# Performance work log

Measured on AMD Instinct MI355X. Metric: run time of the kernel, lower is better.

The kernel has to match this reference:

```python
import jax, jax.numpy as jnp
import numpy as np

B, S, D, H, HD = 4, 2048, 1024, 16, 64  # batch, seq, d_model, heads, head_dim


def setup_inputs() -> dict:
    key = jax.random.key(0)
    ks = jax.random.split(key, 9)
    scale = 0.02
    x = jax.random.normal(ks[0], (B, S, D), jnp.float32)
    Wq = jax.random.normal(ks[1], (D, H, HD), jnp.float32) * scale
    Wk = jax.random.normal(ks[2], (D, H, HD), jnp.float32) * scale
    Wv = jax.random.normal(ks[3], (D, H, HD), jnp.float32) * scale
    bq = jax.random.normal(ks[4], (H, HD), jnp.float32) * scale
    bk = jax.random.normal(ks[5], (H, HD), jnp.float32) * scale
    bv = jax.random.normal(ks[6], (H, HD), jnp.float32) * scale
    Wo = jax.random.normal(ks[7], (H, HD, D), jnp.float32) * scale
    bo = jax.random.normal(ks[8], (D,), jnp.float32) * scale
    return {"x": x, "Wq": Wq, "bq": bq, "Wk": Wk, "bk": bk,
            "Wv": Wv, "bv": bv, "Wo": Wo, "bo": bo}


def reference(x, Wq, bq, Wk, bk, Wv, bv, Wo, bo):
    # QKV projections -> (B, S, H, HD)
    q = jnp.einsum("bsd,dhe->bshe", x, Wq) + bq
    k = jnp.einsum("bsd,dhe->bshe", x, Wk) + bk
    v = jnp.einsum("bsd,dhe->bshe", x, Wv) + bv
    # scaled dot-product attention (deterministic, no mask/bias)
    q = q / jnp.sqrt(jnp.asarray(HD, q.dtype))
    scores = jnp.einsum("bqhd,bkhd->bhqk", q, k)  # (B, H, S, S)
    attn = jax.nn.softmax(scores, axis=-1)
    ctx = jnp.einsum("bhqk,bkhd->bqhd", attn, v)  # (B, S, H, HD)
    # output projection -> (B, S, D)
    return jnp.einsum("bqhd,hdo->bqo", ctx, Wo) + bo
```

## Files before the change

### kernel.cpp

```cpp
#include <hip/hip_runtime.h>


typedef unsigned short u16;
typedef __attribute__((ext_vector_type(4))) float f32x4;
typedef __attribute__((ext_vector_type(8))) short s16x8;
typedef __attribute__((ext_vector_type(4))) unsigned short u16x4;
typedef __attribute__((ext_vector_type(2))) unsigned int u32x2;
typedef __attribute__((ext_vector_type(4))) unsigned int u32x4;

#define DEV __device__ __forceinline__

#if __has_builtin(__builtin_amdgcn_exp2f)
#define EXP2(x) __builtin_amdgcn_exp2f(x)
#else
#define EXP2(x) exp2f(x)
#endif

DEV u16 f2b(float f) {
  unsigned u = __float_as_uint(f);
  u += 0x7fffu + ((u >> 16) & 1u);
  return (u16)(u >> 16);
}

DEV unsigned pack2(float a, float b) {
#if __has_builtin(__builtin_amdgcn_cvt_pk_bf16_f32)
  typedef __attribute__((ext_vector_type(2))) __bf16 bf16x2;
  bf16x2 r = __builtin_amdgcn_cvt_pk_bf16_f32(a, b);
  return __builtin_bit_cast(unsigned, r);
#else
  return (unsigned)f2b(a) | ((unsigned)f2b(b) << 16);
#endif
}

DEV void async16(const void* g, void* l) {
  __builtin_amdgcn_global_load_lds(
      (const __attribute__((address_space(1))) unsigned int*)g,
      (__attribute__((address_space(3))) unsigned int*)l, 16, 0, 0);
}

__global__ void k_cast(const float* __restrict__ x, u16* __restrict__ xb) {
  int i = (blockIdx.x * 256 + threadIdx.x) * 4;
  float4 v = *(const float4*)(x + i);
  u16x4 o;
  o.x = f2b(v.x); o.y = f2b(v.y); o.z = f2b(v.z); o.w = f2b(v.w);
  *(u16x4*)(xb + i) = o;
}

__global__ void k_packw_all(const float* __restrict__ Wq, const float* __restrict__ Wk,
                            const float* __restrict__ Wv, const float* __restrict__ Wo,
                            u16* __restrict__ wt, u16* __restrict__ wot, float qscale) {
  const float* src; u16* dst; float scale = 1.0f;
  switch (blockIdx.z) {
    case 0: src = Wq; dst = wt; scale = qscale; break;
    case 1: src = Wk; dst = wt + 1024 * 1024; break;
    case 2: src = Wv; dst = wt + 2 * 1024 * 1024; break;
    default: src = Wo; dst = wot; break;
  }
  __shared__ float tile[32][33];
  int t = threadIdx.x;
  int k0 = blockIdx.x * 32, n0 = blockIdx.y * 32;
  int c = t & 31, r0 = t >> 5;
#pragma unroll
  for (int p = 0; p < 4; ++p) {
    int r = p * 8 + r0;
    tile[r][c] = src[(size_t)(k0 + r) * 1024 + n0 + c] * scale;
  }
  __syncthreads();
#pragma unroll
  for (int p = 0; p < 4; ++p) {
    int r = p * 8 + r0;
    dst[(size_t)(n0 + r) * 1024 + k0 + c] = f2b(tile[c][r]);
  }
}

__global__ void k_packbias(const float* __restrict__ bq, const float* __restrict__ bk,
                           const float* __restrict__ bv, float* __restrict__ out,
                           float qscale) {
  int t = blockIdx.x * 256 + threadIdx.x;
  float v = (t < 1024) ? bq[t] * qscale : (t < 2048 ? bk[t - 1024] : bv[t - 2048]);
  out[t] = v;
}

template <int MODE>
__global__ __launch_bounds__(256, 2) void k_gemm_bt(
    const u16* __restrict__ A, const u16* __restrict__ Bt,
    const float* __restrict__ bias, void* __restrict__ Cout,
    int K, int ldC, int nbase) {
  __shared__ u16 As[128 * 64];
  __shared__ u16 Bs[128 * 64];
  const int t = threadIdx.x;
  const int w = t >> 6, l = t & 63;
  const int lane15 = l & 15, quad = l >> 4;
  const int m0 = blockIdx.x * 128, n0 = nbase + blockIdx.y * 128;
  const int wm = (w >> 1) * 64, wn = (w & 1) * 64;

  const int srow = t >> 3, cp = t & 7;
  const u16* aSrc[4]; const u16* bSrc[4]; int ldsOff[4];
#pragma unroll
  for (int i = 0; i < 4; ++i) {
    int row = i * 32 + srow;
    int gc = cp ^ (row & 7);
    aSrc[i] = A + (size_t)(m0 + row) * K + gc * 8;
    bSrc[i] = Bt + (size_t)(n0 + row) * K + gc * 8;
    ldsOff[i] = (i * 32 + w * 8) * 64;
  }

  f32x4 acc[4][4] = {};

  for (int kk = 0; kk < K; kk += 64) {
#pragma unroll
    for (int i = 0; i < 4; ++i) async16(aSrc[i] + kk, As + ldsOff[i]);
#pragma unroll
    for (int i = 0; i < 4; ++i) async16(bSrc[i] + kk, Bs + ldsOff[i]);
    __builtin_amdgcn_s_waitcnt(0);
    __syncthreads();

#pragma unroll
    for (int ks = 0; ks < 2; ++ks) {
      s16x8 af[4], bf[4];
#pragma unroll
      for (int mi = 0; mi < 4; ++mi) {
        int r = wm + mi * 16 + lane15;
        int c = ks * 4 + quad;
        af[mi] = *(const s16x8*)(As + r * 64 + (c ^ (r & 7)) * 8);
      }
#pragma unroll
      for (int ni = 0; ni < 4; ++ni) {
        int r = wn + ni * 16 + lane15;
        int c = ks * 4 + quad;
        bf[ni] = *(const s16x8*)(Bs + r * 64 + (c ^ (r & 7)) * 8);
      }
#pragma unroll
      for (int mi = 0; mi < 4; ++mi)
#pragma unroll
        for (int ni = 0; ni < 4; ++ni)
          acc[mi][ni] = (MODE == 2)
              ? __builtin_amdgcn_mfma_f32_16x16x32_bf16(af[mi], bf[ni], acc[mi][ni], 0, 0, 0)
              : __builtin_amdgcn_mfma_f32_16x16x32_bf16(bf[ni], af[mi], acc[mi][ni], 0, 0, 0);
    }
    __syncthreads();
  }

  if (MODE == 2) {
#pragma unroll
    for (int ni = 0; ni < 4; ++ni) {
      int gn = n0 + wn + ni * 16 + lane15;
      float bb = bias[gn];
      int gv = gn - 2048;
      int hh = gv >> 6, hd = gv & 63;
#pragma unroll
      for (int mi = 0; mi < 4; ++mi) {
        int gmBase = m0 + wm + mi * 16 + quad * 4;
        int bb2 = gmBase >> 11, s = gmBase & 2047;
        u32x2 o;
        o.x = pack2(acc[mi][ni][0] + bb, acc[mi][ni][1] + bb);
        o.y = pack2(acc[mi][ni][2] + bb, acc[mi][ni][3] + bb);
        *(u32x2*)((u16*)Cout + (((size_t)(bb2 * 16 + hh) * 64 + hd) * 2048 + s)) = o;
      }
    }
  } else {
#pragma unroll
    for (int ni = 0; ni < 4; ++ni) {
      int gnb = n0 + wn + ni * 16 + quad * 4;
      float4 bb = *(const float4*)(bias + gnb);
#pragma unroll
      for (int mi = 0; mi < 4; ++mi) {
        int gm = m0 + wm + mi * 16 + lane15;
        if (MODE == 0) {
          u32x2 o;
          o.x = pack2(acc[mi][ni][0] + bb.x, acc[mi][ni][1] + bb.y);
          o.y = pack2(acc[mi][ni][2] + bb.z, acc[mi][ni][3] + bb.w);
          *(u32x2*)((u16*)Cout + (size_t)gm * ldC + gnb) = o;
        } else {
          float4 v;
          v.x = acc[mi][ni][0] + bb.x; v.y = acc[mi][ni][1] + bb.y;
          v.z = acc[mi][ni][2] + bb.z; v.w = acc[mi][ni][3] + bb.w;
          *(float4*)((float*)Cout + (size_t)gm * ldC + gnb) = v;
        }
      }
    }
  }
}

__global__ __launch_bounds__(256, 4) void k_flash(
    const u16* __restrict__ qkv, const u16* __restrict__ vt, u16* __restrict__ ctx) {
  __shared__ u16 Ks[128 * 64];
  __shared__ u16 Vs[64 * 128];
  const int t = threadIdx.x;
  const int w = t >> 6, l = t & 63;
  const int lane15 = l & 15, quad = l >> 4;
  const int qt = blockIdx.x, bh = blockIdx.y;
  const int b = bh >> 4, h = bh & 15;

  const int qrow = b * 2048 + qt * 64 + w * 16 + lane15;
  const u16* qp = qkv + (size_t)qrow * 2048 + h * 64 + quad * 8;
  s16x8 qf0 = *(const s16x8*)qp;
  s16x8 qf1 = *(const s16x8*)(qp + 32);

  const int srow = t >> 3, cp = t & 7;
  const u16* kSrc[4]; const u16* vSrc[4]; int ldsOff[4];
#pragma unroll
  for (int i = 0; i < 4; ++i) {
    int krow = i * 32 + srow;
    int xk = (krow & 3) | (((krow >> 3) & 1) << 2);
    kSrc[i] = qkv + (size_t)(b * 2048 + krow) * 2048 + 1024 + h * 64 + (cp ^ xk) * 8;
    int vrow = i * 16 + w * 4 + quad;
    vSrc[i] = vt + (size_t)bh * (64 * 2048) + (size_t)vrow * 2048 + (lane15 ^ (vrow & 7)) * 8;
    ldsOff[i] = (i * 32 + w * 8) * 64;
  }

  const int kr = (lane15 >> 2) * 8 + (lane15 & 3);
  f32x4 O[4] = {};
  f32x4 sacc = {};
  const u32x4 onesu = {0x3F803F80u, 0x3F803F80u, 0x3F803F80u, 0x3F803F80u};
  const s16x8 onesf = __builtin_bit_cast(s16x8, onesu);

  for (int jt = 0; jt < 16; ++jt) {
    const size_t kAdv = (size_t)jt * 128 * 2048;
    const int vAdv = jt * 128;
#pragma unroll
    for (int i = 0; i < 4; ++i) async16(kSrc[i] + kAdv, Ks + ldsOff[i]);
#pragma unroll
    for (int i = 0; i < 4; ++i) async16(vSrc[i] + vAdv, Vs + ldsOff[i]);
    __builtin_amdgcn_s_waitcnt(0);
    __syncthreads();

    f32x4 st[8] = {};
#pragma unroll
    for (int ks2 = 0; ks2 < 2; ++ks2) {
      s16x8 qf = ks2 ? qf1 : qf0;
#pragma unroll
      for (int tt = 0; tt < 8; ++tt) {
        int rr = kr + (tt & 1) * 4 + (tt >> 1) * 32;
        int xk = (rr & 3) | (((rr >> 3) & 1) << 2);
        s16x8 kf = *(const s16x8*)(Ks + rr * 64 + ((ks2 * 4 + quad) ^ xk) * 8);
        st[tt] = __builtin_amdgcn_mfma_f32_16x16x32_bf16(kf, qf, st[tt], 0, 0, 0);
      }
    }

#pragma unroll
    for (int ks = 0; ks < 4; ++ks) {
      float p0 = EXP2(st[2 * ks][0]), p1 = EXP2(st[2 * ks][1]);
      float p2 = EXP2(st[2 * ks][2]), p3 = EXP2(st[2 * ks][3]);
      float p4 = EXP2(st[2 * ks + 1][0]), p5 = EXP2(st[2 * ks + 1][1]);
      float p6 = EXP2(st[2 * ks + 1][2]), p7 = EXP2(st[2 * ks + 1][3]);
      u32x4 pu = {pack2(p0, p1), pack2(p2, p3), pack2(p4, p5), pack2(p6, p7)};
      s16x8 pf = __builtin_bit_cast(s16x8, pu);
      sacc = __builtin_amdgcn_mfma_f32_16x16x32_bf16(onesf, pf, sacc, 0, 0, 0);
#pragma unroll
      for (int co = 0; co < 4; ++co) {
        int rr = co * 16 + lane15;
        s16x8 vf = *(const s16x8*)(Vs + rr * 128 + (((ks * 4 + quad) ^ (rr & 7))) * 8);
        O[co] = __builtin_amdgcn_mfma_f32_16x16x32_bf16(vf, pf, O[co], 0, 0, 0);
      }
    }
    __syncthreads();
  }

  float inv = 1.0f / sacc[0];
#pragma unroll
  for (int co = 0; co < 4; ++co) {
    u32x2 o;
    o.x = pack2(O[co][0] * inv, O[co][1] * inv);
    o.y = pack2(O[co][2] * inv, O[co][3] * inv);
    *(u32x2*)(ctx + (size_t)qrow * 1024 + h * 64 + co * 16 + quad * 4) = o;
  }
}

static constexpr size_t OFF_XB  = 0;
static constexpr size_t OFF_WT  = OFF_XB + (16u << 20);
static constexpr size_t OFF_WOT = OFF_WT + (6u << 20);
static constexpr size_t OFF_B3  = OFF_WOT + (2u << 20);
static constexpr size_t OFF_QKV = OFF_B3 + (1u << 20);
static constexpr size_t OFF_VT  = OFF_QKV + (32u << 20);
static constexpr size_t OFF_CTX = OFF_VT + (16u << 20);

extern "C" void kernel_launch(void* const* d_in, const int* in_sizes, int n_in,
                              void* d_out, int out_size, void* d_ws, size_t ws_size,
                              hipStream_t stream) {
  const float* x  = (const float*)d_in[0];
  const float* Wq = (const float*)d_in[1];
  const float* bq = (const float*)d_in[2];
  const float* Wk = (const float*)d_in[3];
  const float* bk = (const float*)d_in[4];
  const float* Wv = (const float*)d_in[5];
  const float* bv = (const float*)d_in[6];
  const float* Wo = (const float*)d_in[7];
  const float* bo = (const float*)d_in[8];
  char* ws = (char*)d_ws;
  u16* xb    = (u16*)(ws + OFF_XB);
  u16* wt    = (u16*)(ws + OFF_WT);
  u16* wot   = (u16*)(ws + OFF_WOT);
  float* b3  = (float*)(ws + OFF_B3);
  u16* qkv   = (u16*)(ws + OFF_QKV);
  u16* vtb   = (u16*)(ws + OFF_VT);
  u16* ctx   = (u16*)(ws + OFF_CTX);
  float* out = (float*)d_out;

  const float QSCALE = 0.125f * 1.44269504f;

  k_cast<<<8192, 256, 0, stream>>>(x, xb);
  k_packw_all<<<dim3(32, 32, 4), 256, 0, stream>>>(Wq, Wk, Wv, Wo, wt, wot, QSCALE);
  k_packbias<<<12, 256, 0, stream>>>(bq, bk, bv, b3, QSCALE);
  k_gemm_bt<0><<<dim3(64, 16), 256, 0, stream>>>(xb, wt, b3, qkv, 1024, 2048, 0);
  k_gemm_bt<2><<<dim3(64, 8), 256, 0, stream>>>(xb, wt, b3, vtb, 1024, 2048, 2048);
  k_flash<<<dim3(32, 64), 256, 0, stream>>>(qkv, vtb, ctx);
  k_gemm_bt<1><<<dim3(64, 8), 256, 0, stream>>>(ctx, wot, bo, out, 1024, 1024, 0);
}
```

Baseline: 292.2 us.

## Double-buffer flash K/V tiles, stage GEMM epilogues through LDS, reorder grid

The flash kernel now uses 64-key tiles with double-buffered LDS, prefetching the next K/V tile while computing the current one. This removes the trailing barrier and allows 5 blocks per CU. The grid is swapped so that consecutive blocks share the same batch-head. The QK and V-transpose GEMM epilogues now stage through LDS with swizzle so global stores are 16-byte coalesced rows. The fp32 output GEMM switches to transposed MFMA with scalar stores, which may reduce coalescing.

```diff
diff --git a/kernel.cpp b/kernel.cpp
--- a/kernel.cpp
+++ b/kernel.cpp
@@ -84,10 +84,11 @@
 template <int MODE>
 __global__ __launch_bounds__(256, 2) void k_gemm_bt(
     const u16* __restrict__ A, const u16* __restrict__ Bt,
-    const float* __restrict__ bias, void* __restrict__ Cout,
+    const float* __restrict__ bias, void* __restrict__ Cout, u16* __restrict__ VT,
     int K, int ldC, int nbase) {
-  __shared__ u16 As[128 * 64];
-  __shared__ u16 Bs[128 * 64];
+  __shared__ u16 SH[16384];
+  u16* As = SH;
+  u16* Bs = SH + 8192;
   const int t = threadIdx.x;
   const int w = t >> 6, l = t & 63;
   const int lane15 = l & 15, quad = l >> 4;
@@ -134,79 +135,108 @@
       for (int mi = 0; mi < 4; ++mi)
 #pragma unroll
         for (int ni = 0; ni < 4; ++ni)
-          acc[mi][ni] = (MODE == 2)
-              ? __builtin_amdgcn_mfma_f32_16x16x32_bf16(af[mi], bf[ni], acc[mi][ni], 0, 0, 0)
-              : __builtin_amdgcn_mfma_f32_16x16x32_bf16(bf[ni], af[mi], acc[mi][ni], 0, 0, 0);
+          acc[mi][ni] = (MODE == 0)
+              ? __builtin_amdgcn_mfma_f32_16x16x32_bf16(bf[ni], af[mi], acc[mi][ni], 0, 0, 0)
+              : __builtin_amdgcn_mfma_f32_16x16x32_bf16(af[mi], bf[ni], acc[mi][ni], 0, 0, 0);
     }
     __syncthreads();
   }
 
-  if (MODE == 2) {
+  if (MODE == 0) {
+    u16* W = SH + w * 4096;
+#pragma unroll
+    for (int ni = 0; ni < 4; ++ni) {
+      int gnb = n0 + wn + ni * 16 + quad * 4;
+      float4 bb = *(const float4*)(bias + gnb);
+#pragma unroll
+      for (int mi = 0; mi < 4; ++mi) {
+        int mloc = mi * 16 + lane15;
+        int nloc = ni * 16 + quad * 4;
+        int blk = (nloc >> 3) ^ (mloc & 7);
+        u32x2 o;
+        o.x = pack2(acc[mi][ni][0] + bb.x, acc[mi][ni][1] + bb.y);
+        o.y = pack2(acc[mi][ni][2] + bb.z, acc[mi][ni][3] + bb.w);
+        *(u32x2*)(W + mloc * 64 + blk * 8 + (quad & 1) * 4) = o;
+      }
+    }
+    const int l8 = l & 7, lr = l >> 3;
+#pragma unroll
+    for (int it = 0; it < 8; ++it) {
+      int mloc = it * 8 + lr;
+      int lb = l8 ^ (mloc & 7);
+      s16x8 v = *(const s16x8*)(W + mloc * 64 + l8 * 8);
+      int gm = m0 + wm + mloc;
+      *(s16x8*)((u16*)Cout + (size_t)gm * ldC + n0 + wn + lb * 8) = v;
+    }
+  } else if (MODE == 1) {
 #pragma unroll
     for (int ni = 0; ni < 4; ++ni) {
       int gn = n0 + wn + ni * 16 + lane15;
       float bb = bias[gn];
-      int gv = gn - 2048;
-      int hh = gv >> 6, hd = gv & 63;
 #pragma unroll
       for (int mi = 0; mi < 4; ++mi) {
         int gmBase = m0 + wm + mi * 16 + quad * 4;
-        int bb2 = gmBase >> 11, s = gmBase & 2047;
+#pragma unroll
+        for (int r = 0; r < 4; ++r)
+          ((float*)Cout)[(size_t)(gmBase + r) * ldC + gn] = acc[mi][ni][r] + bb;
+      }
+    }
+  } else {
+    u16* W = SH + w * 4096;
+#pragma unroll
+    for (int ni = 0; ni < 4; ++ni) {
+      int gn = n0 + wn + ni * 16 + lane15;
+      float bb = bias[gn];
+#pragma unroll
+      for (int mi = 0; mi < 4; ++mi) {
+        int nloc = ni * 16 + lane15;
+        int mloc = mi * 16 + quad * 4;
+        int blk = (mloc >> 3) ^ (nloc & 7);
         u32x2 o;
         o.x = pack2(acc[mi][ni][0] + bb, acc[mi][ni][1] + bb);
         o.y = pack2(acc[mi][ni][2] + bb, acc[mi][ni][3] + bb);
-        *(u32x2*)((u16*)Cout + (((size_t)(bb2 * 16 + hh) * 64 + hd) * 2048 + s)) = o;
-      }
-    }
-  } else {
-#pragma unroll
-    for (int ni = 0; ni < 4; ++ni) {
-      int gnb = n0 + wn + ni * 16 + quad * 4;
-      float4 bb = *(const float4*)(bias + gnb);
-#pragma unroll
-      for (int mi = 0; mi < 4; ++mi) {
-        int gm = m0 + wm + mi * 16 + lane15;
-        if (MODE == 0) {
-          u32x2 o;
-          o.x = pack2(acc[mi][ni][0] + bb.x, acc[mi][ni][1] + bb.y);
-          o.y = pack2(acc[mi][ni][2] + bb.z, acc[mi][ni][3] + bb.w);
-          *(u32x2*)((u16*)Cout + (size_t)gm * ldC + gnb) = o;
-        } else {
-          float4 v;
-          v.x = acc[mi][ni][0] + bb.x; v.y = acc[mi][ni][1] + bb.y;
-          v.z = acc[mi][ni][2] + bb.z; v.w = acc[mi][ni][3] + bb.w;
-          *(float4*)((float*)Cout + (size_t)gm * ldC + gnb) = v;
-        }
-      }
-    }
-  }
-}
-
-__global__ __launch_bounds__(256, 4) void k_flash(
+        *(u32x2*)(W + nloc * 64 + blk * 8 + (quad & 1) * 4) = o;
+      }
+    }
+    const int l8 = l & 7, lr = l >> 3;
+#pragma unroll
+    for (int it = 0; it < 8; ++it) {
+      int nloc = it * 8 + lr;
+      int lb = l8 ^ (nloc & 7);
+      s16x8 v = *(const s16x8*)(W + nloc * 64 + l8 * 8);
+      int gv = (n0 - 2048) + wn + nloc;
+      int hh = gv >> 6, hd = gv & 63;
+      int gm = m0 + wm + lb * 8;
+      int bb2 = gm >> 11, s = gm & 2047;
+      *(s16x8*)(VT + (((size_t)(bb2 * 16 + hh) * 64 + hd) * 2048 + s)) = v;
+    }
+  }
+}
+
+__global__ __launch_bounds__(256, 5) void k_flash(
     const u16* __restrict__ qkv, const u16* __restrict__ vt, u16* __restrict__ ctx) {
-  __shared__ u16 Ks[128 * 64];
-  __shared__ u16 Vs[64 * 128];
+  __shared__ u16 S[2][8192];
   const int t = threadIdx.x;
   const int w = t >> 6, l = t & 63;
   const int lane15 = l & 15, quad = l >> 4;
-  const int qt = blockIdx.x, bh = blockIdx.y;
+  const int bh = blockIdx.x, qt = blockIdx.y;
   const int b = bh >> 4, h = bh & 15;
 
   const int qrow = b * 2048 + qt * 64 + w * 16 + lane15;
   const u16* qp = qkv + (size_t)qrow * 2048 + h * 64 + quad * 8;
-  s16x8 qf0 = *(const s16x8*)qp;
+  s16x8 qf0 = *(const s16x8*)(qp);
   s16x8 qf1 = *(const s16x8*)(qp + 32);
 
   const int srow = t >> 3, cp = t & 7;
-  const u16* kSrc[4]; const u16* vSrc[4]; int ldsOff[4];
-#pragma unroll
-  for (int i = 0; i < 4; ++i) {
-    int krow = i * 32 + srow;
-    int xk = (krow & 3) | (((krow >> 3) & 1) << 2);
-    kSrc[i] = qkv + (size_t)(b * 2048 + krow) * 2048 + 1024 + h * 64 + (cp ^ xk) * 8;
-    int vrow = i * 16 + w * 4 + quad;
-    vSrc[i] = vt + (size_t)bh * (64 * 2048) + (size_t)vrow * 2048 + (lane15 ^ (vrow & 7)) * 8;
-    ldsOff[i] = (i * 32 + w * 8) * 64;
+  const u16* kSrc[2]; const u16* vSrc[2]; int kOff[2]; int vOff[2];
+#pragma unroll
+  for (int i = 0; i < 2; ++i) {
+    int row = i * 32 + srow;
+    int xk = (row & 3) | (((row >> 3) & 1) << 2);
+    kSrc[i] = qkv + (size_t)(b * 2048 + row) * 2048 + 1024 + h * 64 + (cp ^ xk) * 8;
+    vSrc[i] = vt + (size_t)bh * (64 * 2048) + (size_t)row * 2048 + (cp ^ (row & 7)) * 8;
+    kOff[i] = (i * 32 + w * 8) * 64;
+    vOff[i] = 4096 + (i * 32 + w * 8) * 64;
   }
 
   const int kr = (lane15 >> 2) * 8 + (lane15 & 3);
@@ -215,31 +245,40 @@
   const u32x4 onesu = {0x3F803F80u, 0x3F803F80u, 0x3F803F80u, 0x3F803F80u};
   const s16x8 onesf = __builtin_bit_cast(s16x8, onesu);
 
-  for (int jt = 0; jt < 16; ++jt) {
-    const size_t kAdv = (size_t)jt * 128 * 2048;
-    const int vAdv = jt * 128;
-#pragma unroll
-    for (int i = 0; i < 4; ++i) async16(kSrc[i] + kAdv, Ks + ldsOff[i]);
-#pragma unroll
-    for (int i = 0; i < 4; ++i) async16(vSrc[i] + vAdv, Vs + ldsOff[i]);
+#pragma unroll
+  for (int i = 0; i < 2; ++i) async16(kSrc[i], &S[0][kOff[i]]);
+#pragma unroll
+  for (int i = 0; i < 2; ++i) async16(vSrc[i], &S[0][vOff[i]]);
+
+  for (int jt = 0; jt < 32; ++jt) {
     __builtin_amdgcn_s_waitcnt(0);
     __syncthreads();
-
-    f32x4 st[8] = {};
+    const u16* Sb = S[jt & 1];
+    if (jt < 31) {
+      const size_t kAdv = (size_t)(jt + 1) * 64 * 2048;
+      const int vAdv = (jt + 1) * 64;
+      u16* D = S[(jt & 1) ^ 1];
+#pragma unroll
+      for (int i = 0; i < 2; ++i) async16(kSrc[i] + kAdv, D + kOff[i]);
+#pragma unroll
+      for (int i = 0; i < 2; ++i) async16(vSrc[i] + vAdv, D + vOff[i]);
+    }
+
+    f32x4 st[4] = {};
 #pragma unroll
     for (int ks2 = 0; ks2 < 2; ++ks2) {
       s16x8 qf = ks2 ? qf1 : qf0;
 #pragma unroll
-      for (int tt = 0; tt < 8; ++tt) {
+      for (int tt = 0; tt < 4; ++tt) {
         int rr = kr + (tt & 1) * 4 + (tt >> 1) * 32;
         int xk = (rr & 3) | (((rr >> 3) & 1) << 2);
-        s16x8 kf = *(const s16x8*)(Ks + rr * 64 + ((ks2 * 4 + quad) ^ xk) * 8);
+        s16x8 kf = *(const s16x8*)(Sb + rr * 64 + ((ks2 * 4 + quad) ^ xk) * 8);
         st[tt] = __builtin_amdgcn_mfma_f32_16x16x32_bf16(kf, qf, st[tt], 0, 0, 0);
       }
     }
 
 #pragma unroll
-    for (int ks = 0; ks < 4; ++ks) {
+    for (int ks = 0; ks < 2; ++ks) {
       float p0 = EXP2(st[2 * ks][0]), p1 = EXP2(st[2 * ks][1]);
       float p2 = EXP2(st[2 * ks][2]), p3 = EXP2(st[2 * ks][3]);
       float p4 = EXP2(st[2 * ks + 1][0]), p5 = EXP2(st[2 * ks + 1][1]);
@@ -247,14 +286,15 @@
       u32x4 pu = {pack2(p0, p1), pack2(p2, p3), pack2(p4, p5), pack2(p6, p7)};
       s16x8 pf = __builtin_bit_cast(s16x8, pu);
       sacc = __builtin_amdgcn_mfma_f32_16x16x32_bf16(onesf, pf, sacc, 0, 0, 0);
+      const u16* Vh = Sb + 4096;
+      int c7 = ks * 4 + quad;
 #pragma unroll
       for (int co = 0; co < 4; ++co) {
         int rr = co * 16 + lane15;
-        s16x8 vf = *(const s16x8*)(Vs + rr * 128 + (((ks * 4 + quad) ^ (rr & 7))) * 8);
+        s16x8 vf = *(const s16x8*)(Vh + rr * 64 + ((c7 ^ (rr & 7))) * 8);
         O[co] = __builtin_amdgcn_mfma_f32_16x16x32_bf16(vf, pf, O[co], 0, 0, 0);
       }
     }
-    __syncthreads();
   }
 
   float inv = 1.0f / sacc[0];
@@ -302,8 +342,8 @@
   k_cast<<<8192, 256, 0, stream>>>(x, xb);
   k_packw_all<<<dim3(32, 32, 4), 256, 0, stream>>>(Wq, Wk, Wv, Wo, wt, wot, QSCALE);
   k_packbias<<<12, 256, 0, stream>>>(bq, bk, bv, b3, QSCALE);
-  k_gemm_bt<0><<<dim3(64, 16), 256, 0, stream>>>(xb, wt, b3, qkv, 1024, 2048, 0);
-  k_gemm_bt<2><<<dim3(64, 8), 256, 0, stream>>>(xb, wt, b3, vtb, 1024, 2048, 2048);
-  k_flash<<<dim3(32, 64), 256, 0, stream>>>(qkv, vtb, ctx);
-  k_gemm_bt<1><<<dim3(64, 8), 256, 0, stream>>>(ctx, wot, bo, out, 1024, 1024, 0);
-}
+  k_gemm_bt<0><<<dim3(64, 16), 256, 0, stream>>>(xb, wt, b3, qkv, nullptr, 1024, 2048, 0);
+  k_gemm_bt<2><<<dim3(64, 8), 256, 0, stream>>>(xb, wt, b3, nullptr, vtb, 1024, 2048, 2048);
+  k_flash<<<dim3(64, 32), 256, 0, stream>>>(qkv, vtb, ctx);
+  k_gemm_bt<1><<<dim3(64, 8), 256, 0, stream>>>(ctx, wot, bo, out, nullptr, 1024, 1024, 0);
+}
```

Result: faster. 275.8 us (-5.6%).
